# Kernel tuning notes

Hardware: AMD Instinct MI355X
Metric: run time of the kernel (lower is better)

The kernel has to match this reference:

```python
import jax, jax.numpy as jnp
import numpy as np

D = 12          # tree depth; N = 2**D - 1 = 4095 nodes per tree (heap layout)
B = 64          # batch of trees
V = 128         # VOCAB_SIZE (one-hot token width)
H = 256         # hidden_size
NUM_OPS = 20
TEMP = 3.0      # self.temperature


def setup_inputs() -> dict:
    key = jax.random.key(0)
    ks = jax.random.split(key, 9)
    s = 0.02
    return {
        "arg_hot": jax.random.uniform(ks[0], (B, 2**D - 1, V), dtype=jnp.float32),
        "Wiou": jax.random.normal(ks[1], (V, 3 * H), dtype=jnp.float32) * s,
        "biou": jnp.zeros((3 * H,), jnp.float32),
        "Uiou": jax.random.normal(ks[2], (2, H, 3 * H), dtype=jnp.float32) * s,
        "Wf": jax.random.normal(ks[3], (V, H), dtype=jnp.float32) * s,
        "bf": jnp.zeros((H,), jnp.float32),
        "Uf": jax.random.normal(ks[4], (2, 2, H, H), dtype=jnp.float32) * s,
        "actor_w": jax.random.normal(ks[5], (NUM_OPS, H), dtype=jnp.float32) * s,
        "actor_b": jnp.zeros((NUM_OPS,), jnp.float32),
        "validity_mask": jnp.ones((B, NUM_OPS), jnp.float32),
    }


def _binary_tree_lstm(arg_hot, Wiou, biou, Uiou, Wf, bf, Uf):
    """Levelized apply_binary_lstm: bottom-up N-ary (N=2) Tree-LSTM over a
    complete binary tree stored in heap order (children of node j at level l
    are positions 2j, 2j+1 of level l+1). Missing children (below leaves)
    contribute zero hidden/cell states, matching self.tz in the original."""
    Bn = arg_hot.shape[0]
    h_child = c_child = None
    h = c = None
    for l in reversed(range(D)):
        m = 2 ** l
        x = arg_hot[:, m - 1: 2 * m - 1]                    # [B, m, V]
        if h_child is None:  # leaf level: zero child states
            hk = jnp.zeros((2, Bn, m, H), arg_hot.dtype)
            ck = hk
        else:                # children 2j, 2j+1 are adjacent pairs
            hk = h_child.reshape(Bn, m, 2, H).transpose(2, 0, 1, 3)  # [2,B,m,H]
            ck = c_child.reshape(Bn, m, 2, H).transpose(2, 0, 1, 3)
        iou = (jnp.einsum('bmv,vg->bmg', x, Wiou) + biou
               + jnp.einsum('kbmh,khg->bmg', hk, Uiou))     # [B,m,3H]
        i, o, u = jnp.split(iou, 3, axis=-1)
        i, o, u = jax.nn.sigmoid(i), jax.nn.sigmoid(o), jnp.tanh(u)
        # per-child forget gates f_k = sigma(Wf x + sum_j Uf[k,j] h_j + bf)
        f = jax.nn.sigmoid(jnp.einsum('bmv,vh->bmh', x, Wf) + bf
                           + jnp.einsum('jbmh,kjhd->kbmd', hk, Uf))  # [2,B,m,H]
        c = i * u + jnp.sum(f * ck, axis=0)                 # [B,m,H]
        h = o * jnp.tanh(c)
        h_child, c_child = h, c
    return h[:, 0], c[:, 0]                                  # root states [B,H]


def reference(arg_hot, Wiou, biou, Uiou, Wf, bf, Uf, actor_w, actor_b, validity_mask):
    root_h, _ = _binary_tree_lstm(arg_hot, Wiou, biou, Uiou, Wf, bf, Uf)
    # external-actor branch of policy(): mask weights/bias, add log-mask, tempered softmax
    w = actor_w[None, :, :] * validity_mask[:, :, None]      # [B,O,H]
    b = actor_b[None, :] * validity_mask                     # [B,O]
    logits = jnp.log(validity_mask) + jnp.einsum('bh,boh->bo', root_h, w) + b
    return jax.nn.softmax(logits / TEMP, axis=-1)
```

## Files before the change

kernel.cpp:

```cpp
#include <hip/hip_runtime.h>
#include <hip/hip_bf16.h>
#include <math.h>

typedef __hip_bfloat16 bf16;
typedef float f32x4 __attribute__((ext_vector_type(4)));
typedef short bf16x8 __attribute__((ext_vector_type(8)));

#define NNODES 4095
#define BATCH 64
#define NUM_OPS 20
#define TEMP 3.0f

#define OFF_WBIGT 0x000000ull
#define OFF_BIAS  0x190000ull
#define OFF_HA    0x200000ull
#define OFF_CA    (OFF_HA + (64ull<<20))
#define OFF_HB    (OFF_CA + (64ull<<20))
#define OFF_CB    (OFF_HB + (32ull<<20))

__device__ __forceinline__ float sigmoid_f(float x) {
    return 1.0f / (1.0f + __expf(-x));
}
__device__ __forceinline__ float tanh_f(float x) {
    return 1.0f - 2.0f / (__expf(2.0f * x) + 1.0f);
}

__global__ void init_weights(const float* __restrict__ Wiou,
                             const float* __restrict__ biou,
                             const float* __restrict__ Uiou,
                             const float* __restrict__ Wf,
                             const float* __restrict__ bfv,
                             const float* __restrict__ Uf,
                             bf16* __restrict__ wbigT,
                             float* __restrict__ biasCat)
{
    int idx = blockIdx.x * 256 + threadIdx.x;
    if (idx < 1280 * 640) {
        int k = idx % 640;
        int n = idx / 640;
        int g = n >> 8;
        int ch = n & 255;
        float v;
        if (k < 128) {
            v = (g < 3) ? Wiou[k * 768 + n] : Wf[k * 256 + ch];
        } else {
            int par = (k < 384) ? 0 : 1;
            int hh = (k - 128) & 255;
            if (g < 3) v = Uiou[(par * 256 + hh) * 768 + n];
            else {
                int kk = g - 3;
                v = Uf[(((kk * 2 + par) * 256) + hh) * 256 + ch];
            }
        }
        wbigT[(size_t)n * 640 + k] = __float2bfloat16(v);
    }
    if (idx < 1280) {
        biasCat[idx] = (idx < 768) ? biou[idx] : bfv[idx & 255];
    }
}

template <bool LEAF>
__global__ __launch_bounds__(256, 2)
void level_kernel(const float* __restrict__ arg_hot,
                  const bf16* __restrict__ wbigT,
                  const float* __restrict__ biasCat,
                  const bf16* __restrict__ h_child,
                  const bf16* __restrict__ c_child,
                  bf16* __restrict__ h_out,
                  bf16* __restrict__ c_out,
                  int m, int logm)
{
    constexpr int NG = LEAF ? 3 : 5;
    constexpr int K  = LEAF ? 128 : 640;
    constexpr int BK = 64;
    constexpr int KI = K / BK;

    const int M = BATCH * m;
    const int node_base = m - 1;

    __shared__ bf16 As[128][BK + 8];
    __shared__ bf16 Bs[NG * 32][BK + 8];

    const int tid = threadIdx.x;

    int bid = blockIdx.x;
    int mtiles = gridDim.x >> 3;
    int mtile, chblk;
    if ((mtiles & 7) == 0) {
        int xcd = bid & 7;
        int seq = bid >> 3;
        chblk = seq & 7;
        mtile = ((seq >> 3) << 3) + xcd;
    } else {
        mtile = bid >> 3;
        chblk = bid & 7;
    }
    const int rbase  = mtile * 128;
    const int chbase = chblk * 32;

    const int lane = tid & 63;
    const int wave = tid >> 6;
    const int wr = wave & 1;
    const int wc = wave >> 1;
    const int l15 = lane & 15;
    const int lq  = lane >> 4;

    f32x4 acc[4][NG];
#pragma unroll
    for (int a = 0; a < 4; ++a)
#pragma unroll
        for (int g = 0; g < NG; ++g)
            acc[a][g] = (f32x4){0.f, 0.f, 0.f, 0.f};

    const int a_row0 = tid >> 2;
    const int a_col0 = (tid & 3) * 16;

    for (int kb = 0; kb < KI; ++kb) {
#pragma unroll
        for (int pass = 0; pass < 2; ++pass) {
            int row  = a_row0 + pass * 64;
            int r    = rbase + row;
            int kcol = kb * BK + a_col0;
            int4 w0, w1;
            if (r < M) {
                if (LEAF || kb < 2) {
                    const float* src = arg_hot +
                        ((size_t)(r >> logm) * NNODES + node_base + (r & (m - 1))) * 128 + kcol;
                    alignas(16) bf16 tmp[16];
#pragma unroll
                    for (int u = 0; u < 16; ++u) tmp[u] = __float2bfloat16(src[u]);
                    w0 = *(const int4*)&tmp[0];
                    w1 = *(const int4*)&tmp[8];
                } else {
                    const bf16* src = h_child + (size_t)r * 512 + (kcol - 128);
                    w0 = *(const int4*)src;
                    w1 = *(const int4*)(src + 8);
                }
            } else {
                w0 = make_int4(0, 0, 0, 0);
                w1 = make_int4(0, 0, 0, 0);
            }
            *(int4*)&As[row][a_col0]     = w0;
            *(int4*)&As[row][a_col0 + 8] = w1;
        }
#pragma unroll
        for (int t = 0; t < NG; ++t) {
            int flat = tid + t * 256;
            int brow = flat >> 3;
            int col8 = (flat & 7) * 8;
            int g  = brow >> 5;
            int cl = brow & 31;
            const bf16* src = wbigT + (size_t)(g * 256 + chbase + cl) * 640 + kb * BK + col8;
            *(int4*)&Bs[brow][col8] = *(const int4*)src;
        }
        __syncthreads();
#pragma unroll
        for (int ks = 0; ks < 2; ++ks) {
            int k0 = ks * 32 + lq * 8;
            bf16x8 af[4];
#pragma unroll
            for (int rt = 0; rt < 4; ++rt)
                af[rt] = *(const bf16x8*)&As[wr * 64 + rt * 16 + l15][k0];
#pragma unroll
            for (int g = 0; g < NG; ++g) {
                bf16x8 bfr = *(const bf16x8*)&Bs[g * 32 + wc * 16 + l15][k0];
#pragma unroll
                for (int rt = 0; rt < 4; ++rt)
                    acc[rt][g] = __builtin_amdgcn_mfma_f32_16x16x32_bf16(
                        af[rt], bfr, acc[rt][g], 0, 0, 0);
            }
        }
        __syncthreads();
    }

    const int ch = chbase + wc * 16 + l15;
    const float b_i = biasCat[ch];
    const float b_o = biasCat[256 + ch];
    const float b_u = biasCat[512 + ch];
    const float b_f = LEAF ? 0.f : biasCat[768 + ch];

#pragma unroll
    for (int rt = 0; rt < 4; ++rt) {
#pragma unroll
        for (int ri = 0; ri < 4; ++ri) {
            int r = rbase + wr * 64 + rt * 16 + lq * 4 + ri;
            if (r < M) {
                float i = sigmoid_f(acc[rt][0][ri] + b_i);
                float o = sigmoid_f(acc[rt][1][ri] + b_o);
                float u = tanh_f(acc[rt][2][ri] + b_u);
                float cn;
                if (LEAF) {
                    cn = i * u;
                } else {
                    float f0 = sigmoid_f(acc[rt][3][ri] + b_f);
                    float f1 = sigmoid_f(acc[rt][4][ri] + b_f);
                    float c0 = __bfloat162float(c_child[(size_t)r * 512 + ch]);
                    float c1 = __bfloat162float(c_child[(size_t)r * 512 + 256 + ch]);
                    cn = i * u + f0 * c0 + f1 * c1;
                }
                float h = o * tanh_f(cn);
                h_out[(size_t)r * 256 + ch] = __float2bfloat16(h);
                c_out[(size_t)r * 256 + ch] = __float2bfloat16(cn);
            }
        }
    }
}

__global__ void head_kernel(const bf16* __restrict__ rootH,
                            const float* __restrict__ actor_w,
                            const float* __restrict__ actor_b,
                            const float* __restrict__ vmask,
                            float* __restrict__ out)
{
    int b = blockIdx.x;
    __shared__ float logits[NUM_OPS];
    int t = threadIdx.x;
    if (t < NUM_OPS) {
        const bf16* hr = rootH + b * 256;
        const float* w = actor_w + t * 256;
        float dot = 0.f;
        for (int hh = 0; hh < 256; ++hh)
            dot += __bfloat162float(hr[hh]) * w[hh];
        float mk = vmask[b * NUM_OPS + t];
        float lg = (mk > 0.f) ? (logf(mk) + (dot + actor_b[t]) * mk) : -INFINITY;
        logits[t] = lg / TEMP;
    }
    __syncthreads();
    if (t == 0) {
        float mx = -INFINITY;
        for (int o = 0; o < NUM_OPS; ++o) mx = fmaxf(mx, logits[o]);
        float s = 0.f;
        float e[NUM_OPS];
        for (int o = 0; o < NUM_OPS; ++o) { e[o] = __expf(logits[o] - mx); s += e[o]; }
        float inv = 1.f / s;
        for (int o = 0; o < NUM_OPS; ++o) out[b * NUM_OPS + o] = e[o] * inv;
    }
}

extern "C" void kernel_launch(void* const* d_in, const int* in_sizes, int n_in,
                              void* d_out, int out_size, void* d_ws, size_t ws_size,
                              hipStream_t stream)
{
    const float* arg_hot = (const float*)d_in[0];
    const float* Wiou    = (const float*)d_in[1];
    const float* biou    = (const float*)d_in[2];
    const float* Uiou    = (const float*)d_in[3];
    const float* Wf      = (const float*)d_in[4];
    const float* bfv     = (const float*)d_in[5];
    const float* Uf      = (const float*)d_in[6];
    const float* actor_w = (const float*)d_in[7];
    const float* actor_b = (const float*)d_in[8];
    const float* vmask   = (const float*)d_in[9];

    char* ws = (char*)d_ws;
    bf16*  wbigT   = (bf16*)(ws + OFF_WBIGT);
    float* biasCat = (float*)(ws + OFF_BIAS);
    bf16*  hA = (bf16*)(ws + OFF_HA);
    bf16*  cA = (bf16*)(ws + OFF_CA);
    bf16*  hB = (bf16*)(ws + OFF_HB);
    bf16*  cB = (bf16*)(ws + OFF_CB);

    init_weights<<<dim3((1280 * 640 + 255) / 256), 256, 0, stream>>>(
        Wiou, biou, Uiou, Wf, bfv, Uf, wbigT, biasCat);

    {
        int m = 2048;
        int mtiles = (BATCH * m + 127) / 128;
        level_kernel<true><<<dim3(mtiles * 8), 256, 0, stream>>>(
            arg_hot, wbigT, biasCat, nullptr, nullptr, hA, cA, m, 11);
    }
    for (int l = 10; l >= 0; --l) {
        int m = 1 << l;
        int mtiles = (BATCH * m + 127) / 128;
        bf16 *hc, *cc, *ho, *co;
        if (l & 1) { hc = hB; cc = cB; ho = hA; co = cA; }
        else       { hc = hA; cc = cA; ho = hB; co = cB; }
        level_kernel<false><<<dim3(mtiles * 8), 256, 0, stream>>>(
            arg_hot, wbigT, biasCat, hc, cc, ho, co, m, l);
    }
    head_kernel<<<dim3(BATCH), 64, 0, stream>>>(hB, actor_w, actor_b, vmask, (float*)d_out);
}
```

Measured before the change: 912.7 us.

## Use direct global-to-LDS async loads with chunk-major shared layout

Rewrites the shared-memory staging of the level GEMM. Weight tiles and child hidden states are now copied straight from global memory into LDS through global_load_lds, and LDS is laid out chunk-major ([8][rows][8]) so each wave writes contiguous 16-byte slots. The float input rows are read as float4 and packed to bf16 pairs, and occupancy is raised to 4 blocks per CU. The aim is to cut register round-trips, scalar converts and LDS bank conflicts. The risks are register pressure under the tighter launch bound and the correctness of the async copy addressing; for example, out-of-range rows are no longer zeroed on the h_child path.

```diff
diff --git a/kernel.cpp b/kernel.cpp
--- a/kernel.cpp
+++ b/kernel.cpp
@@ -23,6 +23,13 @@
 }
 __device__ __forceinline__ float tanh_f(float x) {
     return 1.0f - 2.0f / (__expf(2.0f * x) + 1.0f);
+}
+
+__device__ __forceinline__ void async_copy16(const bf16* g, bf16* l) {
+    __builtin_amdgcn_global_load_lds(
+        (const __attribute__((address_space(1))) void*)g,
+        (__attribute__((address_space(3))) void*)l,
+        16, 0, 0);
 }
 
 __global__ void init_weights(const float* __restrict__ Wiou,
@@ -60,7 +67,7 @@
 }
 
 template <bool LEAF>
-__global__ __launch_bounds__(256, 2)
+__global__ __launch_bounds__(256, 4)
 void level_kernel(const float* __restrict__ arg_hot,
                   const bf16* __restrict__ wbigT,
                   const float* __restrict__ biasCat,
@@ -71,15 +78,15 @@
                   int m, int logm)
 {
     constexpr int NG = LEAF ? 3 : 5;
-    constexpr int K  = LEAF ? 128 : 640;
-    constexpr int BK = 64;
-    constexpr int KI = K / BK;
+    constexpr int KI = LEAF ? 2 : 10;
+    constexpr int BROWS = NG * 32;
+    constexpr int BINSTR = (BROWS * 8) / 256;
 
     const int M = BATCH * m;
     const int node_base = m - 1;
 
-    __shared__ bf16 As[128][BK + 8];
-    __shared__ bf16 Bs[NG * 32][BK + 8];
+    __shared__ bf16 As[8][128][8];
+    __shared__ bf16 Bs[8][BROWS][8];
 
     const int tid = threadIdx.x;
 
@@ -112,58 +119,62 @@
         for (int g = 0; g < NG; ++g)
             acc[a][g] = (f32x4){0.f, 0.f, 0.f, 0.f};
 
-    const int a_row0 = tid >> 2;
-    const int a_col0 = (tid & 3) * 16;
+    int boff[BINSTR];
+#pragma unroll
+    for (int i = 0; i < BINSTR; ++i) {
+        int slot  = wave * (BINSTR * 64) + i * 64 + lane;
+        int chunk = slot / BROWS;
+        int brow  = slot % BROWS;
+        int ncol  = (brow >> 5) * 256 + chbase + (brow & 31);
+        boff[i] = ncol * 640 + chunk * 8;
+    }
+
+    const int arow = tid & 127;
+    const int rs = min(rbase + arow, M - 1);
+    const float* xrow = arg_hot +
+        ((size_t)(rs >> logm) * NNODES + node_base + (rs & (m - 1))) * 128;
 
     for (int kb = 0; kb < KI; ++kb) {
-#pragma unroll
-        for (int pass = 0; pass < 2; ++pass) {
-            int row  = a_row0 + pass * 64;
-            int r    = rbase + row;
-            int kcol = kb * BK + a_col0;
-            int4 w0, w1;
-            if (r < M) {
-                if (LEAF || kb < 2) {
-                    const float* src = arg_hot +
-                        ((size_t)(r >> logm) * NNODES + node_base + (r & (m - 1))) * 128 + kcol;
-                    alignas(16) bf16 tmp[16];
-#pragma unroll
-                    for (int u = 0; u < 16; ++u) tmp[u] = __float2bfloat16(src[u]);
-                    w0 = *(const int4*)&tmp[0];
-                    w1 = *(const int4*)&tmp[8];
-                } else {
-                    const bf16* src = h_child + (size_t)r * 512 + (kcol - 128);
-                    w0 = *(const int4*)src;
-                    w1 = *(const int4*)(src + 8);
-                }
-            } else {
-                w0 = make_int4(0, 0, 0, 0);
-                w1 = make_int4(0, 0, 0, 0);
-            }
-            *(int4*)&As[row][a_col0]     = w0;
-            *(int4*)&As[row][a_col0 + 8] = w1;
-        }
-#pragma unroll
-        for (int t = 0; t < NG; ++t) {
-            int flat = tid + t * 256;
-            int brow = flat >> 3;
-            int col8 = (flat & 7) * 8;
-            int g  = brow >> 5;
-            int cl = brow & 31;
-            const bf16* src = wbigT + (size_t)(g * 256 + chbase + cl) * 640 + kb * BK + col8;
-            *(int4*)&Bs[brow][col8] = *(const int4*)src;
+        if (LEAF || kb < 2) {
+            const float* xk = xrow + kb * 64;
+#pragma unroll
+            for (int j = 0; j < 4; ++j) {
+                int chunk = (tid >> 7) + 2 * j;
+                const float* src = xk + chunk * 8;
+                float4 a = *(const float4*)src;
+                float4 b = *(const float4*)(src + 4);
+                union { int4 i4; __hip_bfloat162 h2[4]; } u;
+                u.h2[0] = __float22bfloat162_rn(make_float2(a.x, a.y));
+                u.h2[1] = __float22bfloat162_rn(make_float2(a.z, a.w));
+                u.h2[2] = __float22bfloat162_rn(make_float2(b.x, b.y));
+                u.h2[3] = __float22bfloat162_rn(make_float2(b.z, b.w));
+                *(int4*)&As[chunk][arow][0] = u.i4;
+            }
+        } else {
+            const bf16* abase = h_child + (size_t)(rbase + lane) * 512 + (kb * 64 - 128);
+#pragma unroll
+            for (int i = 0; i < 4; ++i) {
+                int chunk = wave * 2 + (i >> 1);
+                int rowb  = (i & 1) * 64;
+                async_copy16(abase + rowb * 512 + chunk * 8, &As[chunk][rowb][0]);
+            }
+        }
+#pragma unroll
+        for (int i = 0; i < BINSTR; ++i) {
+            const bf16* src = wbigT + boff[i] + kb * 64;
+            bf16* dst = ((bf16*)Bs) + (size_t)(wave * BINSTR + i) * 64 * 8;
+            async_copy16(src, dst);
         }
         __syncthreads();
 #pragma unroll
         for (int ks = 0; ks < 2; ++ks) {
-            int k0 = ks * 32 + lq * 8;
             bf16x8 af[4];
 #pragma unroll
             for (int rt = 0; rt < 4; ++rt)
-                af[rt] = *(const bf16x8*)&As[wr * 64 + rt * 16 + l15][k0];
+                af[rt] = *(const bf16x8*)&As[ks * 4 + lq][wr * 64 + rt * 16 + l15][0];
 #pragma unroll
             for (int g = 0; g < NG; ++g) {
-                bf16x8 bfr = *(const bf16x8*)&Bs[g * 32 + wc * 16 + l15][k0];
+                bf16x8 bfr = *(const bf16x8*)&Bs[ks * 4 + lq][g * 32 + wc * 16 + l15][0];
 #pragma unroll
                 for (int rt = 0; rt < 4; ++rt)
                     acc[rt][g] = __builtin_amdgcn_mfma_f32_16x16x32_bf16(
```

After: 1.107 ms. 1.21x slower.

## Load MFMA fragments directly from global memory with fragment-ordered weights and register double buffering

Applied to the files above, without the earlier changes.

Drops the LDS staging and __syncthreads in the level GEMM. Each wave now loads its A fragments straight from arg_hot or h_child, and its B fragments from weights pre-permuted into MFMA fragment order (with a separate compact leaf copy). Fragment loads are double-buffered in registers. Blocks grow to 512 threads covering 256 rows. This removes LDS round-trips and barriers, but the same weight and activation data is now re-read from global or L2 by multiple waves, and register pressure rises.

```diff
diff --git a/kernel.cpp b/kernel.cpp
--- a/kernel.cpp
+++ b/kernel.cpp
@@ -11,8 +11,9 @@
 #define NUM_OPS 20
 #define TEMP 3.0f
 
-#define OFF_WBIGT 0x000000ull
-#define OFF_BIAS  0x190000ull
+#define OFF_WTI   0x000000ull
+#define OFF_WTL   0x1A0000ull
+#define OFF_BIAS  0x1D8000ull
 #define OFF_HA    0x200000ull
 #define OFF_CA    (OFF_HA + (64ull<<20))
 #define OFF_HB    (OFF_CA + (64ull<<20))
@@ -31,7 +32,8 @@
                              const float* __restrict__ Wf,
                              const float* __restrict__ bfv,
                              const float* __restrict__ Uf,
-                             bf16* __restrict__ wbigT,
+                             bf16* __restrict__ wtI,
+                             bf16* __restrict__ wtL,
                              float* __restrict__ biasCat)
 {
     int idx = blockIdx.x * 256 + threadIdx.x;
@@ -52,7 +54,18 @@
                 v = Uf[(((kk * 2 + par) * 256) + hh) * 256 + ch];
             }
         }
-        wbigT[(size_t)n * 640 + k] = __float2bfloat16(v);
+        bf16 bv = __float2bfloat16(v);
+        int chblk = ch >> 5;
+        int cl    = ch & 31;
+        int kb    = k >> 6;
+        int chunk = (k & 63) >> 3;
+        int e     = k & 7;
+        size_t dI = (((size_t)(chblk * 10 + kb) * 8 + chunk) * 160 + g * 32 + cl) * 8 + e;
+        wtI[dI] = bv;
+        if (k < 128 && g < 3) {
+            size_t dL = (((size_t)(chblk * 2 + kb) * 8 + chunk) * 96 + g * 32 + cl) * 8 + e;
+            wtL[dL] = bv;
+        }
     }
     if (idx < 1280) {
         biasCat[idx] = (idx < 768) ? biou[idx] : bfv[idx & 255];
@@ -60,9 +73,9 @@
 }
 
 template <bool LEAF>
-__global__ __launch_bounds__(256, 2)
+__global__ __launch_bounds__(512, 2)
 void level_kernel(const float* __restrict__ arg_hot,
-                  const bf16* __restrict__ wbigT,
+                  const bf16* __restrict__ wt,
                   const float* __restrict__ biasCat,
                   const bf16* __restrict__ h_child,
                   const bf16* __restrict__ c_child,
@@ -71,15 +84,11 @@
                   int m, int logm)
 {
     constexpr int NG = LEAF ? 3 : 5;
-    constexpr int K  = LEAF ? 128 : 640;
-    constexpr int BK = 64;
-    constexpr int KI = K / BK;
+    constexpr int KI = LEAF ? 2 : 10;
+    constexpr int BR = LEAF ? 96 : 160;
 
     const int M = BATCH * m;
     const int node_base = m - 1;
-
-    __shared__ bf16 As[128][BK + 8];
-    __shared__ bf16 Bs[NG * 32][BK + 8];
 
     const int tid = threadIdx.x;
 
@@ -95,13 +104,13 @@
         mtile = bid >> 3;
         chblk = bid & 7;
     }
-    const int rbase  = mtile * 128;
+    const int rbase  = mtile * 256;
     const int chbase = chblk * 32;
 
     const int lane = tid & 63;
     const int wave = tid >> 6;
-    const int wr = wave & 1;
-    const int wc = wave >> 1;
+    const int wr = wave & 3;
+    const int wc = wave >> 2;
     const int l15 = lane & 15;
     const int lq  = lane >> 4;
 
@@ -112,65 +121,65 @@
         for (int g = 0; g < NG; ++g)
             acc[a][g] = (f32x4){0.f, 0.f, 0.f, 0.f};
 
-    const int a_row0 = tid >> 2;
-    const int a_col0 = (tid & 3) * 16;
-
+    const float* xptr[4];
+    const bf16*  hptr[4];
+#pragma unroll
+    for (int rt = 0; rt < 4; ++rt) {
+        int row = rbase + wr * 64 + rt * 16 + l15;
+        row = min(row, M - 1);
+        xptr[rt] = arg_hot +
+            ((size_t)(row >> logm) * NNODES + node_base + (row & (m - 1))) * 128;
+        hptr[rt] = LEAF ? (const bf16*)nullptr : h_child + (size_t)row * 512;
+    }
+    const bf16* bptr = wt + (size_t)chblk * (KI * 8 * BR * 8)
+                          + ((size_t)lq * BR + wc * 16 + l15) * 8;
+
+    bf16x8 fa[2][4];
+    bf16x8 fb[2][NG];
+
+    auto load_set = [&](int kb, int ks, int buf) {
+        if (!LEAF && kb >= 2) {
+            int off = (kb * 64 - 128) + ks * 32 + lq * 8;
+#pragma unroll
+            for (int rt = 0; rt < 4; ++rt)
+                fa[buf][rt] = *(const bf16x8*)(hptr[rt] + off);
+        } else {
+            int off = kb * 64 + ks * 32 + lq * 8;
+#pragma unroll
+            for (int rt = 0; rt < 4; ++rt) {
+                const float* s = xptr[rt] + off;
+                float4 u0 = *(const float4*)s;
+                float4 u1 = *(const float4*)(s + 4);
+                union { bf16x8 v; __hip_bfloat162 h2[4]; } cv;
+                cv.h2[0] = __float22bfloat162_rn(make_float2(u0.x, u0.y));
+                cv.h2[1] = __float22bfloat162_rn(make_float2(u0.z, u0.w));
+                cv.h2[2] = __float22bfloat162_rn(make_float2(u1.x, u1.y));
+                cv.h2[3] = __float22bfloat162_rn(make_float2(u1.z, u1.w));
+                fa[buf][rt] = cv.v;
+            }
+        }
+        size_t base = ((size_t)kb * 8 + ks * 4) * BR * 8;
+#pragma unroll
+        for (int g = 0; g < NG; ++g)
+            fb[buf][g] = *(const bf16x8*)(bptr + base + (size_t)g * 32 * 8);
+    };
+
+    load_set(0, 0, 0);
+#pragma unroll
     for (int kb = 0; kb < KI; ++kb) {
 #pragma unroll
-        for (int pass = 0; pass < 2; ++pass) {
-            int row  = a_row0 + pass * 64;
-            int r    = rbase + row;
-            int kcol = kb * BK + a_col0;
-            int4 w0, w1;
-            if (r < M) {
-                if (LEAF || kb < 2) {
-                    const float* src = arg_hot +
-                        ((size_t)(r >> logm) * NNODES + node_base + (r & (m - 1))) * 128 + kcol;
-                    alignas(16) bf16 tmp[16];
-#pragma unroll
-                    for (int u = 0; u < 16; ++u) tmp[u] = __float2bfloat16(src[u]);
-                    w0 = *(const int4*)&tmp[0];
-                    w1 = *(const int4*)&tmp[8];
-                } else {
-                    const bf16* src = h_child + (size_t)r * 512 + (kcol - 128);
-                    w0 = *(const int4*)src;
-                    w1 = *(const int4*)(src + 8);
-                }
-            } else {
-                w0 = make_int4(0, 0, 0, 0);
-                w1 = make_int4(0, 0, 0, 0);
-            }
-            *(int4*)&As[row][a_col0]     = w0;
-            *(int4*)&As[row][a_col0 + 8] = w1;
-        }
-#pragma unroll
-        for (int t = 0; t < NG; ++t) {
-            int flat = tid + t * 256;
-            int brow = flat >> 3;
-            int col8 = (flat & 7) * 8;
-            int g  = brow >> 5;
-            int cl = brow & 31;
-            const bf16* src = wbigT + (size_t)(g * 256 + chbase + cl) * 640 + kb * BK + col8;
-            *(int4*)&Bs[brow][col8] = *(const int4*)src;
-        }
-        __syncthreads();
-#pragma unroll
         for (int ks = 0; ks < 2; ++ks) {
-            int k0 = ks * 32 + lq * 8;
-            bf16x8 af[4];
-#pragma unroll
-            for (int rt = 0; rt < 4; ++rt)
-                af[rt] = *(const bf16x8*)&As[wr * 64 + rt * 16 + l15][k0];
-#pragma unroll
-            for (int g = 0; g < NG; ++g) {
-                bf16x8 bfr = *(const bf16x8*)&Bs[g * 32 + wc * 16 + l15][k0];
+            int p = (kb * 2 + ks) & 1;
+            int nkb = (ks == 1) ? kb + 1 : kb;
+            int nks = ks ^ 1;
+            if (nkb < KI) load_set(nkb, nks, p ^ 1);
+#pragma unroll
+            for (int g = 0; g < NG; ++g)
 #pragma unroll
                 for (int rt = 0; rt < 4; ++rt)
                     acc[rt][g] = __builtin_amdgcn_mfma_f32_16x16x32_bf16(
-                        af[rt], bfr, acc[rt][g], 0, 0, 0);
-            }
-        }
-        __syncthreads();
+                        fa[p][rt], fb[p][g], acc[rt][g], 0, 0, 0);
+        }
     }
 
     const int ch = chbase + wc * 16 + l15;
@@ -253,7 +262,8 @@
     const float* vmask   = (const float*)d_in[9];
 
     char* ws = (char*)d_ws;
-    bf16*  wbigT   = (bf16*)(ws + OFF_WBIGT);
+    bf16*  wtI     = (bf16*)(ws + OFF_WTI);
+    bf16*  wtL     = (bf16*)(ws + OFF_WTL);
     float* biasCat = (float*)(ws + OFF_BIAS);
     bf16*  hA = (bf16*)(ws + OFF_HA);
     bf16*  cA = (bf16*)(ws + OFF_CA);
@@ -261,22 +271,22 @@
     bf16*  cB = (bf16*)(ws + OFF_CB);
 
     init_weights<<<dim3((1280 * 640 + 255) / 256), 256, 0, stream>>>(
-        Wiou, biou, Uiou, Wf, bfv, Uf, wbigT, biasCat);
+        Wiou, biou, Uiou, Wf, bfv, Uf, wtI, wtL, biasCat);
 
     {
         int m = 2048;
-        int mtiles = (BATCH * m + 127) / 128;
-        level_kernel<true><<<dim3(mtiles * 8), 256, 0, stream>>>(
-            arg_hot, wbigT, biasCat, nullptr, nullptr, hA, cA, m, 11);
+        int mtiles = (BATCH * m + 255) / 256;
+        level_kernel<true><<<dim3(mtiles * 8), 512, 0, stream>>>(
+            arg_hot, wtL, biasCat, nullptr, nullptr, hA, cA, m, 11);
     }
     for (int l = 10; l >= 0; --l) {
         int m = 1 << l;
-        int mtiles = (BATCH * m + 127) / 128;
+        int mtiles = (BATCH * m + 255) / 256;
         bf16 *hc, *cc, *ho, *co;
         if (l & 1) { hc = hB; cc = cB; ho = hA; co = cA; }
         else       { hc = hA; cc = cA; ho = hB; co = cB; }
-        level_kernel<false><<<dim3(mtiles * 8), 256, 0, stream>>>(
-            arg_hot, wbigT, biasCat, hc, cc, ho, co, m, l);
+        level_kernel<false><<<dim3(mtiles * 8), 512, 0, stream>>>(
+            arg_hot, wtI, biasCat, hc, cc, ho, co, m, l);
     }
     head_kernel<<<dim3(BATCH), 64, 0, stream>>>(hB, actor_w, actor_b, vmask, (float*)d_out);
 }
```

Result: slower. 1.375 ms (+50.7%).
